# Kernel tuning notes

Hardware: AMD Instinct MI355X
Metric: run time of the kernel (lower is better)

## Reference

```python
import jax, jax.numpy as jnp
import numpy as np

B, S, E, DK = 8, 2048, 1024, 64


def setup_inputs() -> dict:
    key = jax.random.key(0)
    ks = jax.random.split(key, 10)
    inv_e = 1.0 / np.sqrt(E)
    return {
        "k": jax.random.normal(ks[0], (B, S, E), dtype=jnp.float32),
        "q": jax.random.normal(ks[1], (B, S, E), dtype=jnp.float32),
        "v": jax.random.normal(ks[2], (B, S, E), dtype=jnp.float32),
        "mask": jax.random.randint(ks[3], (B, S, S), 0, 2, dtype=jnp.int32),
        "w_q": jax.random.uniform(ks[4], (DK, E), jnp.float32, -inv_e, inv_e),
        "b_q": jax.random.uniform(ks[5], (DK,), jnp.float32, -inv_e, inv_e),
        "w_k": jax.random.uniform(ks[6], (DK, E), jnp.float32, -inv_e, inv_e),
        "b_k": jax.random.uniform(ks[7], (DK,), jnp.float32, -inv_e, inv_e),
        "w_v": jax.random.uniform(ks[8], (DK, E), jnp.float32, -inv_e, inv_e),
        "b_v": jax.random.uniform(ks[9], (DK,), jnp.float32, -inv_e, inv_e),
    }


def reference(k, q, v, mask, w_q, b_q, w_k, b_k, w_v, b_v):
    # Linear projections: x @ W^T + b  -> [B, S, DK]
    K = jnp.einsum('bse,de->bsd', k, w_k) + b_k
    Q = jnp.einsum('bse,de->bsd', q, w_q) + b_q
    V = jnp.einsum('bse,de->bsd', v, w_v) + b_v
    scale = 1.0 / jnp.sqrt(jnp.asarray(DK, dtype=Q.dtype))
    scores = jnp.einsum('bqd,bkd->bqk', Q, K) * scale  # [B, S, S]
    scores = jnp.where(mask == 0, jnp.asarray(-1e9, scores.dtype), scores)
    attention_weights = jax.nn.softmax(scores, axis=2)
    attention_scores = jnp.einsum('bqk,bkd->bqd', attention_weights, V)
    return attention_scores, attention_weights
```

## Files before the change

### kernel.cpp

```cpp
#include <hip/hip_runtime.h>
#include <math.h>
#include <stdint.h>

#define BB 8
#define SS 2048
#define EE 1024
#define DKK 64

typedef _Float16 half8 __attribute__((ext_vector_type(8)));
typedef float floatx4 __attribute__((ext_vector_type(4)));

__device__ __forceinline__ void split8(float4 a, float4 b, half8& hi, half8& lo) {
  float va[8] = {a.x, a.y, a.z, a.w, b.x, b.y, b.z, b.w};
#pragma unroll
  for (int j = 0; j < 8; ++j) {
    _Float16 h = (_Float16)va[j];
    hi[j] = h;
    lo[j] = (_Float16)(va[j] - (float)h);
  }
}

__global__ __launch_bounds__(256, 3) void proj_kernel(
    const float* __restrict__ q_in, const float* __restrict__ k_in,
    const float* __restrict__ v_in,
    const float* __restrict__ w_q, const float* __restrict__ b_q,
    const float* __restrict__ w_k, const float* __restrict__ b_k,
    const float* __restrict__ w_v, const float* __restrict__ b_v,
    _Float16* __restrict__ Qh, _Float16* __restrict__ Kh,
    _Float16* __restrict__ VhT) {
  const int which = blockIdx.y;
  const float* X = which == 0 ? q_in : (which == 1 ? k_in : v_in);
  const float* W = which == 0 ? w_q : (which == 1 ? w_k : w_v);
  const float* bias = which == 0 ? b_q : (which == 1 ? b_k : b_v);

  __shared__ __align__(16) char Xh[64 * 128];
  __shared__ __align__(16) char Xl[64 * 128];
  __shared__ __align__(16) char Wh[64 * 128];
  __shared__ __align__(16) char Wl[64 * 128];

  const int t = threadIdx.x;
  const int row0 = blockIdx.x * 64;
  const int sr = t >> 2;
  const int c4 = t & 3;
  const int l = t & 63;
  const int li = l & 15, g = l >> 4;
  const int w = t >> 6;

  const float* xbase = X + (size_t)(row0 + sr) * EE + c4 * 16;
  const float* wbase = W + (size_t)sr * EE + c4 * 16;

  float4 xr[4], wr[4];
#pragma unroll
  for (int u = 0; u < 4; ++u) {
    xr[u] = ((const float4*)xbase)[u];
    wr[u] = ((const float4*)wbase)[u];
  }

  floatx4 acc[4];
#pragma unroll
  for (int c = 0; c < 4; ++c) acc[c] = (floatx4){0.f, 0.f, 0.f, 0.f};

  const int xrow_off = (w * 16 + li) * 128;
  const int swz = li & 7;

  for (int e0 = 0; e0 < EE; e0 += 64) {
    half8 xh0, xl0, xh1, xl1, wh0, wl0, wh1, wl1;
    split8(xr[0], xr[1], xh0, xl0);
    split8(xr[2], xr[3], xh1, xl1);
    split8(wr[0], wr[1], wh0, wl0);
    split8(wr[2], wr[3], wh1, wl1);
    __syncthreads();
    {
      const int p0 = ((c4 * 2 + 0) ^ (sr & 7)) * 16;
      const int p1 = ((c4 * 2 + 1) ^ (sr & 7)) * 16;
      *(half8*)(Xh + sr * 128 + p0) = xh0;
      *(half8*)(Xh + sr * 128 + p1) = xh1;
      *(half8*)(Xl + sr * 128 + p0) = xl0;
      *(half8*)(Xl + sr * 128 + p1) = xl1;
      *(half8*)(Wh + sr * 128 + p0) = wh0;
      *(half8*)(Wh + sr * 128 + p1) = wh1;
      *(half8*)(Wl + sr * 128 + p0) = wl0;
      *(half8*)(Wl + sr * 128 + p1) = wl1;
    }
    if (e0 + 64 < EE) {
#pragma unroll
      for (int u = 0; u < 4; ++u) {
        xr[u] = ((const float4*)(xbase + e0 + 64))[u];
        wr[u] = ((const float4*)(wbase + e0 + 64))[u];
      }
    }
    __syncthreads();
    half8 axh[2], axl[2];
#pragma unroll
    for (int h = 0; h < 2; ++h) {
      const int apos = ((h * 4 + g) ^ swz) * 16;
      axh[h] = *(const half8*)(Xh + xrow_off + apos);
      axl[h] = *(const half8*)(Xl + xrow_off + apos);
    }
#pragma unroll
    for (int c = 0; c < 4; ++c) {
      const int brow_off = (c * 16 + li) * 128;
#pragma unroll
      for (int h = 0; h < 2; ++h) {
        const int bpos = ((h * 4 + g) ^ swz) * 16;
        half8 bh = *(const half8*)(Wh + brow_off + bpos);
        half8 bl = *(const half8*)(Wl + brow_off + bpos);
        acc[c] = __builtin_amdgcn_mfma_f32_16x16x32_f16(axh[h], bh, acc[c], 0, 0, 0);
        acc[c] = __builtin_amdgcn_mfma_f32_16x16x32_f16(axh[h], bl, acc[c], 0, 0, 0);
        acc[c] = __builtin_amdgcn_mfma_f32_16x16x32_f16(axl[h], bh, acc[c], 0, 0, 0);
      }
    }
  }

  float bvv[4];
#pragma unroll
  for (int c = 0; c < 4; ++c) bvv[c] = bias[c * 16 + li];

  if (which < 2) {
    _Float16* P = (which == 0) ? Qh : Kh;
#pragma unroll
    for (int c = 0; c < 4; ++c)
#pragma unroll
      for (int r = 0; r < 4; ++r)
        P[(size_t)(row0 + w * 16 + g * 4 + r) * DKK + c * 16 + li] =
            (_Float16)(acc[c][r] + bvv[c]);
  } else {
    const int bb = row0 >> 11;
    const int s0 = row0 & (SS - 1);
#pragma unroll
    for (int c = 0; c < 4; ++c)
#pragma unroll
      for (int r = 0; r < 4; ++r)
        VhT[((size_t)bb * DKK + c * 16 + li) * SS + s0 + w * 16 + g * 4 + r] =
            (_Float16)(acc[c][r] + bvv[c]);
  }
}

__global__ __launch_bounds__(512, 4) void flash_kernel(
    const _Float16* __restrict__ Qh, const _Float16* __restrict__ Kh,
    const _Float16* __restrict__ VhT, const int* __restrict__ mask,
    float* __restrict__ outsc, uint32_t* __restrict__ mbits_g,
    float* __restrict__ mstats) {
  __shared__ __align__(16) char Klds[16384];
  __shared__ __align__(16) char Vlds[16384];
  __shared__ uint32_t mwords[32][66];
  __shared__ float Obuf[32][68];
  __shared__ float mlbuf[8][16][2];
  __shared__ float lstat[32][2];

  const int t = threadIdx.x;
  const int b = (int)blockIdx.x & 7;
  const int q0 = ((int)blockIdx.x >> 3) * 32;
  const int l = t & 63;
  const int li = l & 15, g = l >> 4;
  const int w = t >> 6;
  const int qh = w & 1, ws = w >> 1;
  const float SCALE = 0.125f;

  {
    const int* mp = mask + ((size_t)b * SS + q0) * SS;
    for (int j = 0; j < 128; ++j) {
      const int flat = j * 512 + t;
      const int mz = (mp[flat] != 0);
      unsigned long long bal = __ballot(mz);
      if ((l & 31) == 0) {
        const uint32_t val = (uint32_t)(bal >> l);
        const int word = flat >> 5;
        const int qq = word >> 6, wc = word & 63;
        mwords[qq][wc] = val;
        mbits_g[((size_t)(b * SS + q0 + qq)) * 64 + wc] = val;
      }
    }
  }

  half8 aq[2];
  {
    const _Float16* qp = Qh + ((size_t)b * SS + q0 + qh * 16 + li) * DKK;
    aq[0] = *(const half8*)(qp + g * 8);
    aq[1] = *(const half8*)(qp + 32 + g * 8);
  }

  float m_c = -3.0e38f, l_c = 0.f;
  floatx4 O[4];
#pragma unroll
  for (int d = 0; d < 4; ++d) O[d] = (floatx4){0.f, 0.f, 0.f, 0.f};

  __syncthreads();

  for (int kt = 0; kt < 16; ++kt) {
    half8 kv[2], vv[2];
#pragma unroll
    for (int p = 0; p < 2; ++p) {
      const int slot = t + p * 512;
      const int kr = slot >> 3, kc = slot & 7;
      kv[p] = *(const half8*)(Kh + ((size_t)b * SS + kt * 128 + kr) * DKK +
                              ((kc ^ (kr & 7)) * 8));
      const int vd = slot >> 4, vc = slot & 15;
      vv[p] = *(const half8*)(VhT + ((size_t)b * DKK + vd) * SS + kt * 128 +
                              ((vc ^ (vd & 7)) * 8));
    }
    __syncthreads();
#pragma unroll
    for (int p = 0; p < 2; ++p) {
      const int slot = t + p * 512;
      *(half8*)(Klds + slot * 16) = kv[p];
      *(half8*)(Vlds + slot * 16) = vv[p];
    }
    __syncthreads();

    floatx4 sc[2];
#pragma unroll
    for (int cb = 0; cb < 2; ++cb) {
      const int krow = ws * 32 + cb * 16 + li;
      const int rs = krow & 7;
      floatx4 acc = {0.f, 0.f, 0.f, 0.f};
#pragma unroll
      for (int h = 0; h < 2; ++h) {
        half8 ka = *(const half8*)(Klds + krow * 128 + (((h * 4 + g) ^ rs) * 16));
        acc = __builtin_amdgcn_mfma_f32_16x16x32_f16(ka, aq[h], acc, 0, 0, 0);
      }
      sc[cb] = acc;
    }

    const uint32_t mw = mwords[qh * 16 + li][kt * 4 + ws];
    float p[2][4];
    float tmax = -3.0e38f;
#pragma unroll
    for (int cb = 0; cb < 2; ++cb)
#pragma unroll
      for (int r = 0; r < 4; ++r) {
        const float s =
            ((mw >> (cb * 16 + g * 4 + r)) & 1u) ? sc[cb][r] * SCALE : -1.0e9f;
        p[cb][r] = s;
        tmax = fmaxf(tmax, s);
      }
    tmax = fmaxf(tmax, __shfl_xor(tmax, 16));
    tmax = fmaxf(tmax, __shfl_xor(tmax, 32));
    const float m_new = fmaxf(m_c, tmax);
    const float alpha = __expf(m_c - m_new);
    m_c = m_new;
    float lsum = 0.f;
#pragma unroll
    for (int cb = 0; cb < 2; ++cb)
#pragma unroll
      for (int r = 0; r < 4; ++r) {
        p[cb][r] = __expf(p[cb][r] - m_new);
        lsum += p[cb][r];
      }
    l_c = l_c * alpha + lsum;

    half8 pB;
#pragma unroll
    for (int j = 0; j < 4; ++j) {
      pB[j] = (_Float16)p[0][j];
      pB[4 + j] = (_Float16)p[1][j];
    }

#pragma unroll
    for (int dblk = 0; dblk < 4; ++dblk) {
      const int d = dblk * 16 + li;
      const int rowb = d * 256;
      const int c1 = ws * 4 + (g >> 1);
      const int c2 = c1 + 2;
      const int sub = (g & 1) * 8;
      uint2 a1 = *(const uint2*)(Vlds + rowb + ((c1 ^ (li & 7)) * 16) + sub);
      uint2 a2 = *(const uint2*)(Vlds + rowb + ((c2 ^ (li & 7)) * 16) + sub);
      half8 av;
      *(uint2*)&av = a1;
      *((uint2*)&av + 1) = a2;
      O[dblk] = O[dblk] * alpha;
      O[dblk] = __builtin_amdgcn_mfma_f32_16x16x32_f16(av, pB, O[dblk], 0, 0, 0);
    }
  }

  l_c += __shfl_xor(l_c, 16);
  l_c += __shfl_xor(l_c, 32);
  if (g == 0) {
    mlbuf[w][li][0] = m_c;
    mlbuf[w][li][1] = l_c;
  }
  __syncthreads();
  float mstar = -3.0e38f;
#pragma unroll
  for (int p2 = 0; p2 < 4; ++p2)
    mstar = fmaxf(mstar, mlbuf[p2 * 2 + qh][li][0]);
  float lstar = 0.f;
#pragma unroll
  for (int p2 = 0; p2 < 4; ++p2)
    lstar += mlbuf[p2 * 2 + qh][li][1] * __expf(mlbuf[p2 * 2 + qh][li][0] - mstar);
  const float fown = __expf(m_c - mstar);
  if (g == 0 && ws == 0) {
    lstat[qh * 16 + li][0] = mstar;
    lstat[qh * 16 + li][1] = 1.f / lstar;
  }
#pragma unroll
  for (int dblk = 0; dblk < 4; ++dblk) O[dblk] = O[dblk] * fown;

  for (int ph = 0; ph < 4; ++ph) {
    if (ws == ph) {
      const int qq = qh * 16 + li;
#pragma unroll
      for (int dblk = 0; dblk < 4; ++dblk)
#pragma unroll
        for (int r = 0; r < 4; ++r) {
          const int d = dblk * 16 + g * 4 + r;
          if (ph == 0)
            Obuf[qq][d] = O[dblk][r];
          else
            Obuf[qq][d] += O[dblk][r];
        }
    }
    __syncthreads();
  }

  {
    const int qq = t >> 4;
    const int d0 = (t & 15) * 4;
    const float rl = lstat[qq][1];
    float4 o;
    o.x = Obuf[qq][d0 + 0] * rl;
    o.y = Obuf[qq][d0 + 1] * rl;
    o.z = Obuf[qq][d0 + 2] * rl;
    o.w = Obuf[qq][d0 + 3] * rl;
    *(float4*)(outsc + ((size_t)(b * SS + q0 + qq)) * DKK + d0) = o;
  }
  if (t < 32) {
    mstats[((size_t)(b * SS + q0 + t)) * 2 + 0] = lstat[t][0];
    mstats[((size_t)(b * SS + q0 + t)) * 2 + 1] = lstat[t][1];
  }
}

__global__ __launch_bounds__(512, 4) void weights_kernel(
    const _Float16* __restrict__ Qh, const _Float16* __restrict__ Kh,
    const uint32_t* __restrict__ mbits_g, const float* __restrict__ mstats,
    float* __restrict__ wts) {
  __shared__ __align__(16) char Klds[16384];

  const int t = threadIdx.x;
  const int b = (int)blockIdx.x & 7;
  const int q0 = ((int)blockIdx.x >> 3) * 32;
  const int l = t & 63;
  const int li = l & 15, g = l >> 4;
  const int w = t >> 6;
  const int qh = w & 1, cq = w >> 1;
  const float SCALE = 0.125f;

  half8 aq[2];
  {
    const _Float16* qp = Qh + ((size_t)b * SS + q0 + qh * 16 + li) * DKK;
    aq[0] = *(const half8*)(qp + g * 8);
    aq[1] = *(const half8*)(qp + 32 + g * 8);
  }
  float mr[4], rl[4];
#pragma unroll
  for (int r = 0; r < 4; ++r) {
    const size_t q = (size_t)b * SS + q0 + qh * 16 + g * 4 + r;
    mr[r] = mstats[q * 2 + 0];
    rl[r] = mstats[q * 2 + 1];
  }

  for (int kt = 0; kt < 16; ++kt) {
    half8 kv[2];
#pragma unroll
    for (int p = 0; p < 2; ++p) {
      const int slot = t + p * 512;
      const int kr = slot >> 3, kc = slot & 7;
      kv[p] = *(const half8*)(Kh + ((size_t)b * SS + kt * 128 + kr) * DKK +
                              ((kc ^ (kr & 7)) * 8));
    }
    uint32_t mw[4];
#pragma unroll
    for (int r = 0; r < 4; ++r)
      mw[r] = mbits_g[((size_t)(b * SS + q0 + qh * 16 + g * 4 + r)) * 64 +
                      kt * 4 + cq];
    __syncthreads();
#pragma unroll
    for (int p = 0; p < 2; ++p) {
      const int slot = t + p * 512;
      *(half8*)(Klds + slot * 16) = kv[p];
    }
    __syncthreads();
#pragma unroll
    for (int cb = 0; cb < 2; ++cb) {
      const int krow = cq * 32 + cb * 16 + li;
      const int rs = krow & 7;
      floatx4 acc = {0.f, 0.f, 0.f, 0.f};
#pragma unroll
      for (int h = 0; h < 2; ++h) {
        half8 kb = *(const half8*)(Klds + krow * 128 + (((h * 4 + g) ^ rs) * 16));
        acc = __builtin_amdgcn_mfma_f32_16x16x32_f16(aq[h], kb, acc, 0, 0, 0);
      }
#pragma unroll
      for (int r = 0; r < 4; ++r) {
        const float wv = ((mw[r] >> (cb * 16 + li)) & 1u)
                             ? __expf(acc[r] * SCALE - mr[r]) * rl[r]
                             : 0.f;
        wts[((size_t)(b * SS + q0 + qh * 16 + g * 4 + r)) * SS + kt * 128 +
            cq * 32 + cb * 16 + li] = wv;
      }
    }
  }
}

extern "C" void kernel_launch(void* const* d_in, const int* in_sizes, int n_in,
                              void* d_out, int out_size, void* d_ws, size_t ws_size,
                              hipStream_t stream) {
  (void)in_sizes; (void)n_in; (void)out_size; (void)ws_size;
  const float* k_in = (const float*)d_in[0];
  const float* q_in = (const float*)d_in[1];
  const float* v_in = (const float*)d_in[2];
  const int* mask = (const int*)d_in[3];
  const float* w_q = (const float*)d_in[4];
  const float* b_q = (const float*)d_in[5];
  const float* w_k = (const float*)d_in[6];
  const float* b_k = (const float*)d_in[7];
  const float* w_v = (const float*)d_in[8];
  const float* b_v = (const float*)d_in[9];

  float* out_scores = (float*)d_out;
  float* out_weights = out_scores + (size_t)BB * SS * DKK;

  char* wsp = (char*)d_ws;
  const size_t nBSD = (size_t)BB * SS * DKK;
  _Float16* Qh = (_Float16*)wsp;
  _Float16* Kh = (_Float16*)(wsp + nBSD * 2);
  _Float16* VhT = (_Float16*)(wsp + nBSD * 4);
  uint32_t* mbits_g = (uint32_t*)(wsp + nBSD * 6);
  float* mstats = (float*)(wsp + nBSD * 6 + (size_t)BB * SS * 64 * 4);

  proj_kernel<<<dim3(256, 3), 256, 0, stream>>>(q_in, k_in, v_in, w_q, b_q,
                                                w_k, b_k, w_v, b_v, Qh, Kh, VhT);
  flash_kernel<<<512, 512, 0, stream>>>(Qh, Kh, VhT, mask, out_scores,
                                        mbits_g, mstats);
  weights_kernel<<<512, 512, 0, stream>>>(Qh, Kh, mbits_g, mstats, out_weights);
}
```

Before: 187.4 us.

## Load K fragments directly from global, prefetch V tiles, vectorize mask packing

Both the flash and weights kernels now read K operand fragments straight from global/L2 into registers instead of staging them through LDS, removing the K shared buffer and two barriers per tile in the weights kernel. The flash kernel prefetches the next V tile into registers while the current one is consumed from LDS. Mask bit-packing now uses per-thread int4 loads and a single vector store of packed words, replacing the ballot-based loop. This trades LDS traffic and barriers for more global load instructions and some register pressure, and the weights kernel drops its occupancy hint in launch bounds.

```diff
diff --git a/kernel.cpp b/kernel.cpp
--- a/kernel.cpp
+++ b/kernel.cpp
@@ -141,7 +141,6 @@
     const _Float16* __restrict__ VhT, const int* __restrict__ mask,
     float* __restrict__ outsc, uint32_t* __restrict__ mbits_g,
     float* __restrict__ mstats) {
-  __shared__ __align__(16) char Klds[16384];
   __shared__ __align__(16) char Vlds[16384];
   __shared__ uint32_t mwords[32][66];
   __shared__ float Obuf[32][68];
@@ -159,18 +158,25 @@
 
   {
     const int* mp = mask + ((size_t)b * SS + q0) * SS;
-    for (int j = 0; j < 128; ++j) {
-      const int flat = j * 512 + t;
-      const int mz = (mp[flat] != 0);
-      unsigned long long bal = __ballot(mz);
-      if ((l & 31) == 0) {
-        const uint32_t val = (uint32_t)(bal >> l);
-        const int word = flat >> 5;
-        const int qq = word >> 6, wc = word & 63;
-        mwords[qq][wc] = val;
-        mbits_g[((size_t)(b * SS + q0 + qq)) * 64 + wc] = val;
-      }
-    }
+    uint32_t wbuf[4];
+#pragma unroll
+    for (int u = 0; u < 4; ++u) {
+      const int word = t * 4 + u;
+      const int4* src = (const int4*)(mp + word * 32);
+      uint32_t bits = 0;
+#pragma unroll
+      for (int c = 0; c < 8; ++c) {
+        int4 m4 = src[c];
+        bits |= (uint32_t)(m4.x != 0) << (c * 4 + 0);
+        bits |= (uint32_t)(m4.y != 0) << (c * 4 + 1);
+        bits |= (uint32_t)(m4.z != 0) << (c * 4 + 2);
+        bits |= (uint32_t)(m4.w != 0) << (c * 4 + 3);
+      }
+      wbuf[u] = bits;
+      mwords[word >> 6][word & 63] = bits;
+    }
+    *(uint4*)(mbits_g + ((size_t)(b * SS + q0)) * 64 + t * 4) =
+        *(const uint4*)wbuf;
   }
 
   half8 aq[2];
@@ -185,40 +191,47 @@
 #pragma unroll
   for (int d = 0; d < 4; ++d) O[d] = (floatx4){0.f, 0.f, 0.f, 0.f};
 
-  __syncthreads();
+  half8 vv[2];
+#pragma unroll
+  for (int p = 0; p < 2; ++p) {
+    const int slot = t + p * 512;
+    const int vd = slot >> 4, vc = slot & 15;
+    vv[p] = *(const half8*)(VhT + ((size_t)b * DKK + vd) * SS +
+                            ((vc ^ (vd & 7)) * 8));
+  }
+
+  const _Float16* kbase = Kh + (size_t)b * SS * DKK;
 
   for (int kt = 0; kt < 16; ++kt) {
-    half8 kv[2], vv[2];
-#pragma unroll
-    for (int p = 0; p < 2; ++p) {
-      const int slot = t + p * 512;
-      const int kr = slot >> 3, kc = slot & 7;
-      kv[p] = *(const half8*)(Kh + ((size_t)b * SS + kt * 128 + kr) * DKK +
-                              ((kc ^ (kr & 7)) * 8));
-      const int vd = slot >> 4, vc = slot & 15;
-      vv[p] = *(const half8*)(VhT + ((size_t)b * DKK + vd) * SS + kt * 128 +
-                              ((vc ^ (vd & 7)) * 8));
-    }
     __syncthreads();
 #pragma unroll
-    for (int p = 0; p < 2; ++p) {
-      const int slot = t + p * 512;
-      *(half8*)(Klds + slot * 16) = kv[p];
-      *(half8*)(Vlds + slot * 16) = vv[p];
-    }
+    for (int p = 0; p < 2; ++p)
+      *(half8*)(Vlds + (t + p * 512) * 16) = vv[p];
     __syncthreads();
-
-    floatx4 sc[2];
+    if (kt + 1 < 16) {
+#pragma unroll
+      for (int p = 0; p < 2; ++p) {
+        const int slot = t + p * 512;
+        const int vd = slot >> 4, vc = slot & 15;
+        vv[p] = *(const half8*)(VhT + ((size_t)b * DKK + vd) * SS +
+                                (kt + 1) * 128 + ((vc ^ (vd & 7)) * 8));
+      }
+    }
+
+    half8 ka[2][2];
 #pragma unroll
     for (int cb = 0; cb < 2; ++cb) {
       const int krow = ws * 32 + cb * 16 + li;
-      const int rs = krow & 7;
+      const _Float16* kp = kbase + (size_t)(kt * 128 + krow) * DKK;
+      ka[cb][0] = *(const half8*)(kp + g * 8);
+      ka[cb][1] = *(const half8*)(kp + 32 + g * 8);
+    }
+    floatx4 sc[2];
+#pragma unroll
+    for (int cb = 0; cb < 2; ++cb) {
       floatx4 acc = {0.f, 0.f, 0.f, 0.f};
-#pragma unroll
-      for (int h = 0; h < 2; ++h) {
-        half8 ka = *(const half8*)(Klds + krow * 128 + (((h * 4 + g) ^ rs) * 16));
-        acc = __builtin_amdgcn_mfma_f32_16x16x32_f16(ka, aq[h], acc, 0, 0, 0);
-      }
+      acc = __builtin_amdgcn_mfma_f32_16x16x32_f16(ka[cb][0], aq[0], acc, 0, 0, 0);
+      acc = __builtin_amdgcn_mfma_f32_16x16x32_f16(ka[cb][1], aq[1], acc, 0, 0, 0);
       sc[cb] = acc;
     }
 
@@ -330,12 +343,10 @@
   }
 }
 
-__global__ __launch_bounds__(512, 4) void weights_kernel(
+__global__ __launch_bounds__(512) void weights_kernel(
     const _Float16* __restrict__ Qh, const _Float16* __restrict__ Kh,
     const uint32_t* __restrict__ mbits_g, const float* __restrict__ mstats,
     float* __restrict__ wts) {
-  __shared__ __align__(16) char Klds[16384];
-
   const int t = threadIdx.x;
   const int b = (int)blockIdx.x & 7;
   const int q0 = ((int)blockIdx.x >> 3) * 32;
@@ -358,38 +369,27 @@
     mr[r] = mstats[q * 2 + 0];
     rl[r] = mstats[q * 2 + 1];
   }
+  const _Float16* kbase = Kh + (size_t)b * SS * DKK;
 
   for (int kt = 0; kt < 16; ++kt) {
-    half8 kv[2];
-#pragma unroll
-    for (int p = 0; p < 2; ++p) {
-      const int slot = t + p * 512;
-      const int kr = slot >> 3, kc = slot & 7;
-      kv[p] = *(const half8*)(Kh + ((size_t)b * SS + kt * 128 + kr) * DKK +
-                              ((kc ^ (kr & 7)) * 8));
-    }
     uint32_t mw[4];
 #pragma unroll
     for (int r = 0; r < 4; ++r)
       mw[r] = mbits_g[((size_t)(b * SS + q0 + qh * 16 + g * 4 + r)) * 64 +
                       kt * 4 + cq];
-    __syncthreads();
-#pragma unroll
-    for (int p = 0; p < 2; ++p) {
-      const int slot = t + p * 512;
-      *(half8*)(Klds + slot * 16) = kv[p];
-    }
-    __syncthreads();
+    half8 kb[2][2];
 #pragma unroll
     for (int cb = 0; cb < 2; ++cb) {
       const int krow = cq * 32 + cb * 16 + li;
-      const int rs = krow & 7;
+      const _Float16* kp = kbase + (size_t)(kt * 128 + krow) * DKK;
+      kb[cb][0] = *(const half8*)(kp + g * 8);
+      kb[cb][1] = *(const half8*)(kp + 32 + g * 8);
+    }
+#pragma unroll
+    for (int cb = 0; cb < 2; ++cb) {
       floatx4 acc = {0.f, 0.f, 0.f, 0.f};
-#pragma unroll
-      for (int h = 0; h < 2; ++h) {
-        half8 kb = *(const half8*)(Klds + krow * 128 + (((h * 4 + g) ^ rs) * 16));
-        acc = __builtin_amdgcn_mfma_f32_16x16x32_f16(aq[h], kb, acc, 0, 0, 0);
-      }
+      acc = __builtin_amdgcn_mfma_f32_16x16x32_f16(aq[0], kb[cb][0], acc, 0, 0, 0);
+      acc = __builtin_amdgcn_mfma_f32_16x16x32_f16(aq[1], kb[cb][1], acc, 0, 0, 0);
 #pragma unroll
       for (int r = 0; r < 4; ++r) {
         const float wv = ((mw[r] >> (cb * 16 + li)) & 1u)
```

Result: no change. 184.2 us (-1.7%).
